# Optimization experiments

Hardware: AMD Instinct MI355X
Metric: run time of the kernel (lower is better)

## Reference

```python
import jax, jax.numpy as jnp
import numpy as np

SQRT_DK = np.sqrt(512.0).astype(np.float32)


def setup_inputs() -> dict:
    key = jax.random.key(0)
    k1, k2, k3 = jax.random.split(key, 3)
    x = jax.random.normal(k1, (16, 2048, 512), dtype=jnp.float32)
    W1 = jax.random.normal(k2, (512, 10), dtype=jnp.float32) * 0.05
    W2 = jax.random.normal(k3, (10, 512), dtype=jnp.float32) * 0.05
    return {"x": x, "W1": W1, "W2": W2}


def reference(x, W1, W2):
    # x: [B, A, D]; low-rank bilinear scores: (x@W1) @ (W2@x^T) -> [B, A, A]
    B, A, D = x.shape
    left = jnp.einsum('bad,dr->bar', x, W1)          # [B, A, 10]
    right = jnp.einsum('rd,bcd->brc', W2, x)         # [B, 10, A]
    scores = jnp.einsum('bar,brc->bac', left, right)  # [B, A, A]
    attn = jax.nn.softmax(scores / SQRT_DK, axis=-1)
    out = jnp.einsum('bac,bcd->bad', attn, x)         # requires_value=True
    return out
```

## Files before the change

### kernel.cpp

```cpp
#include <hip/hip_runtime.h>
#include <cstdint>
#include <cstddef>


typedef float    f32x4 __attribute__((ext_vector_type(4)));
typedef _Float16 half8 __attribute__((ext_vector_type(8)));
typedef _Float16 half4 __attribute__((ext_vector_type(4)));
typedef _Float16 half2 __attribute__((ext_vector_type(2)));

#define B_  16
#define A_  2048
#define D_  512
#define SCALE 0.04419417382415922f

__global__ __launch_bounds__(256) void k01_prep(const float* __restrict__ x,
                                                const float* __restrict__ W1,
                                                const float* __restrict__ W2,
                                                _Float16* __restrict__ xT,
                                                float* __restrict__ left,
                                                _Float16* __restrict__ rightT) {
    __shared__ float xs[64 * 64];
    __shared__ _Float16 Wc[32 * 520];
    int t = threadIdx.x;
    for (int i = t; i < 2560; i += 256) {
        int r = i >> 8, d = (i & 255) << 1;
        half2 h;
        h[0] = (_Float16)(W1[d * 10 + r] * SCALE);
        h[1] = (_Float16)(W1[(d + 1) * 10 + r] * SCALE);
        *(half2*)&Wc[r * 520 + d] = h;
    }
    for (int i = t; i < 2560; i += 256) {
        int r = i >> 8, d = (i & 255) << 1;
        half2 h;
        h[0] = (_Float16)W2[r * 512 + d];
        h[1] = (_Float16)W2[r * 512 + d + 1];
        *(half2*)&Wc[(16 + r) * 520 + d] = h;
    }
    for (int i = t; i < 3120; i += 256) {
        int rz = i / 260, dw = i % 260;
        int row = rz < 6 ? 10 + rz : 20 + rz;
        *(uint32_t*)&Wc[row * 520 + dw * 2] = 0u;
    }

    int bid = blockIdx.x;
    int b = bid >> 5, rg = bid & 31;
    int c0 = rg << 6;
    const float* xb = x + ((size_t)(b * A_ + c0)) * D_;
    int lane = t & 63, w = t >> 6, quad = lane >> 4, col = lane & 15;
    f32x4 accA = {0.f, 0.f, 0.f, 0.f}, accB = {0.f, 0.f, 0.f, 0.f};

    for (int dc = 0; dc < 8; ++dc) {
        int d0 = dc << 6;
        __syncthreads();
#pragma unroll
        for (int j = 0; j < 4; ++j) {
            int idx = t + 256 * j;
            int c = idx >> 4, ch = idx & 15;
            float4 v = *(const float4*)(xb + (size_t)c * D_ + d0 + ch * 4);
            *(float4*)&xs[c * 64 + ((ch ^ (c & 15)) << 2)] = v;
        }
        __syncthreads();
        _Float16* xo = xT + ((size_t)b * D_ + d0) * A_ + c0;
#pragma unroll
        for (int j = 0; j < 4; ++j) {
            int idx = t + 256 * j;
            int d = idx >> 4, cq = (idx & 15) << 2;
            int ch = d >> 2, e = d & 3;
            half4 h;
#pragma unroll
            for (int k = 0; k < 4; ++k) {
                int c = cq + k;
                h[k] = (_Float16)xs[c * 64 + ((ch ^ (c & 15)) << 2) + e];
            }
            *(half4*)(xo + (size_t)d * A_ + cq) = h;
        }
#pragma unroll
        for (int kt = 0; kt < 2; ++kt) {
            int kk = kt * 32 + quad * 8;
            int r = w * 16 + col;
            int ch0 = kk >> 2;
            float4 v0 = *(const float4*)&xs[r * 64 + ((ch0 ^ col) << 2)];
            float4 v1 = *(const float4*)&xs[r * 64 + (((ch0 + 1) ^ col) << 2)];
            half8 af;
            af[0] = (_Float16)v0.x; af[1] = (_Float16)v0.y; af[2] = (_Float16)v0.z; af[3] = (_Float16)v0.w;
            af[4] = (_Float16)v1.x; af[5] = (_Float16)v1.y; af[6] = (_Float16)v1.z; af[7] = (_Float16)v1.w;
            int k = d0 + kk;
            half8 bf0 = *(const half8*)&Wc[col * 520 + k];
            half8 bf1 = *(const half8*)&Wc[(col + 16) * 520 + k];
            accA = __builtin_amdgcn_mfma_f32_16x16x32_f16(af, bf0, accA, 0, 0, 0);
            accB = __builtin_amdgcn_mfma_f32_16x16x32_f16(af, bf1, accB, 0, 0, 0);
        }
    }
#pragma unroll
    for (int q = 0; q < 4; ++q) {
        size_t grow = (size_t)bid * 64 + w * 16 + quad * 4 + q;
        if (col < 10) left[grow * 10 + col] = accA[q];
        if (col < 12) rightT[grow * 12 + col] = (_Float16)accB[q];
    }
}

__global__ __launch_bounds__(256, 2) void k3_attn(const _Float16* __restrict__ xT,
                                                  const float* __restrict__ left,
                                                  const _Float16* __restrict__ rightT,
                                                  float* __restrict__ out) {
    __shared__ _Float16 XTl[256 * 32];
    __shared__ _Float16 Ps[128 * 40];
    __shared__ _Float16 rl[32 * 40];
    __shared__ float rowsum[128];
    int t = threadIdx.x, lane = t & 63, w = t >> 6;
    int quad = lane >> 4, c16 = lane & 15;
    int bid = blockIdx.x;
    int nb = bid & 1, at = (bid >> 1) & 15, b = bid >> 5;
    int a0 = at << 7, n0 = nb << 8;
    int waveM = w & 1, waveN = w >> 1;

    for (int i = t; i < 320; i += 256) {
        int c = i / 10, dw = i % 10;
        *(uint32_t*)((char*)rl + c * 80 + 24 + dw * 4) = 0u;
    }

    half8 lf[2];
#pragma unroll
    for (int i = 0; i < 2; ++i) {
        int arow = a0 + (2 * w + i) * 16 + c16;
        const float* lp = left + (size_t)((b << 11) + arow) * 10;
#pragma unroll
        for (int j = 0; j < 8; ++j) {
            int r = quad * 8 + j;
            lf[i][j] = (r < 10) ? (_Float16)lp[r] : (_Float16)0.f;
        }
    }

    f32x4 acc[4][8];
#pragma unroll
    for (int mi = 0; mi < 4; ++mi)
#pragma unroll
        for (int ni = 0; ni < 8; ++ni) acc[mi][ni] = (f32x4){0.f, 0.f, 0.f, 0.f};
    float psum[2][4] = {{0.f, 0.f, 0.f, 0.f}, {0.f, 0.f, 0.f, 0.f}};

    const _Float16* xTb = xT + ((size_t)b * D_ + n0) * A_;
    const _Float16* rTb = rightT + (size_t)(b << 11) * 12;

    int psA[4];
#pragma unroll
    for (int mi = 0; mi < 4; ++mi) psA[mi] = (waveM * 64 + mi * 16 + c16) * 80 + quad * 16;
    int xtB[8];
#pragma unroll
    for (int ni = 0; ni < 8; ++ni) {
        int nr = waveN * 128 + ni * 16 + c16;
        xtB[ni] = nr * 64 + ((quad ^ ((nr >> 1) & 3)) << 4);
    }
    int rlB[2];
#pragma unroll
    for (int kh = 0; kh < 2; ++kh) rlB[kh] = (kh * 16 + c16) * 80 + quad * 16;

    int nloc0 = w * 64 + (lane >> 2);
    int kq = lane & 3;

    for (int kt = 0; kt < 64; ++kt) {
        int c0 = kt << 5;
        __syncthreads();
        if (t < 192) {
            int c = t / 6, dw = t % 6;
            uint32_t v = *(const uint32_t*)((const char*)(rTb + (size_t)(c0 + c) * 12) + dw * 4);
            *(uint32_t*)((char*)rl + c * 80 + dw * 4) = v;
        }
#pragma unroll
        for (int cc = 0; cc < 4; ++cc) {
            int nl = nloc0 + cc * 16;
            int kqs = kq ^ ((nl >> 1) & 3);
            const _Float16* src = xTb + (size_t)nl * A_ + c0 + kqs * 8;
            _Float16* dst = &XTl[(w * 64 + cc * 16) * 32];
            __builtin_amdgcn_global_load_lds((const __attribute__((address_space(1))) void*)src,
                                             (__attribute__((address_space(3))) void*)dst,
                                             16, 0, 0);
        }
        __syncthreads();
#pragma unroll
        for (int kh = 0; kh < 2; ++kh) {
            half8 bfr = *(const half8*)((const char*)rl + rlB[kh]);
#pragma unroll
            for (int i = 0; i < 2; ++i) {
                f32x4 z = {0.f, 0.f, 0.f, 0.f};
                f32x4 pc = __builtin_amdgcn_mfma_f32_16x16x32_f16(lf[i], bfr, z, 0, 0, 0);
#pragma unroll
                for (int q = 0; q < 4; ++q) {
                    float p = __expf(pc[q]);
                    psum[i][q] += p;
                    Ps[((2 * w + i) * 16 + quad * 4 + q) * 40 + kh * 16 + c16] = (_Float16)p;
                }
            }
        }
        __syncthreads();
        half8 af[4], bf[8];
#pragma unroll
        for (int mi = 0; mi < 4; ++mi) af[mi] = *(const half8*)((const char*)Ps + psA[mi]);
#pragma unroll
        for (int ni = 0; ni < 8; ++ni) bf[ni] = *(const half8*)((const char*)XTl + xtB[ni]);
#pragma unroll
        for (int mi = 0; mi < 4; ++mi)
#pragma unroll
            for (int ni = 0; ni < 8; ++ni)
                acc[mi][ni] = __builtin_amdgcn_mfma_f32_16x16x32_f16(af[mi], bf[ni], acc[mi][ni], 0, 0, 0);
    }

#pragma unroll
    for (int i = 0; i < 2; ++i)
#pragma unroll
        for (int q = 0; q < 4; ++q) {
            float s = psum[i][q];
            s += __shfl_xor(s, 1);
            s += __shfl_xor(s, 2);
            s += __shfl_xor(s, 4);
            s += __shfl_xor(s, 8);
            if (c16 == 0) rowsum[(2 * w + i) * 16 + quad * 4 + q] = s;
        }
    __syncthreads();

    float* ob = out + ((size_t)b * A_ + a0) * D_ + n0;
#pragma unroll
    for (int mi = 0; mi < 4; ++mi) {
#pragma unroll
        for (int q = 0; q < 4; ++q) {
            int ar = waveM * 64 + mi * 16 + quad * 4 + q;
            float sc = 1.0f / rowsum[ar];
#pragma unroll
            for (int ni = 0; ni < 8; ++ni)
                ob[(size_t)ar * D_ + waveN * 128 + ni * 16 + c16] = acc[mi][ni][q] * sc;
        }
    }
}

extern "C" void kernel_launch(void* const* d_in, const int* in_sizes, int n_in,
                              void* d_out, int out_size, void* d_ws, size_t ws_size,
                              hipStream_t stream) {
    const float* x  = (const float*)d_in[0];
    const float* W1 = (const float*)d_in[1];
    const float* W2 = (const float*)d_in[2];
    float* out = (float*)d_out;
    char* ws = (char*)d_ws;
    _Float16* xT    = (_Float16*)ws;
    float*    left  = (float*)(ws + 33554432);
    _Float16* rightT= (_Float16*)(ws + 34865152);

    k01_prep<<<512, 256, 0, stream>>>(x, W1, W2, xT, left, rightT);
    k3_attn<<<512, 256, 0, stream>>>(xT, left, rightT, out);
}
```

Before: 233.7 us.

## Retile attention and prep kernels, prepack weights, use exp2 softmax

Weight conversion moves into a small separate kernel that writes MFMA-ready fp16 fragments. The prep kernel now uses 32-row tiles with a split-K reduction across wave pairs, and the attention kernel uses 128-wide output tiles with 64-column K steps, occupancy 3, and a grid remap to improve L2 locality. The scale is folded into exp2 with log2e, and the Ps buffer is doubled per K half. This gives more blocks and less per-block weight setup, but it recomputes the score MFMAs for each of the four column tiles and adds a third kernel launch.

```diff
diff --git a/kernel.cpp b/kernel.cpp
--- a/kernel.cpp
+++ b/kernel.cpp
@@ -5,117 +5,128 @@
 
 typedef float    f32x4 __attribute__((ext_vector_type(4)));
 typedef _Float16 half8 __attribute__((ext_vector_type(8)));
-typedef _Float16 half4 __attribute__((ext_vector_type(4)));
-typedef _Float16 half2 __attribute__((ext_vector_type(2)));
 
 #define B_  16
 #define A_  2048
 #define D_  512
-#define SCALE 0.04419417382415922f
+#define KSCALE 0.06375872f
+
+__device__ inline float fast_exp2(float v) {
+#if __has_builtin(__builtin_amdgcn_exp2f)
+    return __builtin_amdgcn_exp2f(v);
+#else
+    return __expf(v * 0.6931471805599453f);
+#endif
+}
+
+__global__ __launch_bounds__(256) void kw_prep(const float* __restrict__ W1,
+                                               const float* __restrict__ W2,
+                                               _Float16* __restrict__ Wf) {
+    int pi = blockIdx.x * 256 + threadIdx.x;
+    int kt = pi >> 6, lane = pi & 63;
+    int quad = lane >> 4, col = lane & 15;
+    half8 h1, h2;
+#pragma unroll
+    for (int j = 0; j < 8; ++j) {
+        int d = kt * 32 + quad * 8 + j;
+        h1[j] = (col < 10) ? (_Float16)(W1[d * 10 + col] * KSCALE) : (_Float16)0.f;
+        h2[j] = (col < 12) ? (_Float16)W2[col * 512 + d] : (_Float16)0.f;
+    }
+    *(half8*)(Wf + (size_t)pi * 16) = h1;
+    *(half8*)(Wf + (size_t)pi * 16 + 8) = h2;
+}
 
 __global__ __launch_bounds__(256) void k01_prep(const float* __restrict__ x,
-                                                const float* __restrict__ W1,
-                                                const float* __restrict__ W2,
+                                                const _Float16* __restrict__ Wf,
                                                 _Float16* __restrict__ xT,
                                                 float* __restrict__ left,
                                                 _Float16* __restrict__ rightT) {
-    __shared__ float xs[64 * 64];
-    __shared__ _Float16 Wc[32 * 520];
-    int t = threadIdx.x;
-    for (int i = t; i < 2560; i += 256) {
-        int r = i >> 8, d = (i & 255) << 1;
-        half2 h;
-        h[0] = (_Float16)(W1[d * 10 + r] * SCALE);
-        h[1] = (_Float16)(W1[(d + 1) * 10 + r] * SCALE);
-        *(half2*)&Wc[r * 520 + d] = h;
-    }
-    for (int i = t; i < 2560; i += 256) {
-        int r = i >> 8, d = (i & 255) << 1;
-        half2 h;
-        h[0] = (_Float16)W2[r * 512 + d];
-        h[1] = (_Float16)W2[r * 512 + d + 1];
-        *(half2*)&Wc[(16 + r) * 520 + d] = h;
-    }
-    for (int i = t; i < 3120; i += 256) {
-        int rz = i / 260, dw = i % 260;
-        int row = rz < 6 ? 10 + rz : 20 + rz;
-        *(uint32_t*)&Wc[row * 520 + dw * 2] = 0u;
-    }
-
+    __shared__ float xs[32 * 64];
+    int t = threadIdx.x, lane = t & 63, w = t >> 6;
+    int quad = lane >> 4, c16 = lane & 15;
     int bid = blockIdx.x;
-    int b = bid >> 5, rg = bid & 31;
-    int c0 = rg << 6;
-    const float* xb = x + ((size_t)(b * A_ + c0)) * D_;
-    int lane = t & 63, w = t >> 6, quad = lane >> 4, col = lane & 15;
+    int b = bid >> 6, grp = bid & 63;
+    int c0 = grp << 5;
+    const float* xb = x + ((size_t)b * A_ + c0) * D_;
+    int tile = w >> 1, kki = w & 1;
+    int ar = tile * 16 + c16;
     f32x4 accA = {0.f, 0.f, 0.f, 0.f}, accB = {0.f, 0.f, 0.f, 0.f};
 
     for (int dc = 0; dc < 8; ++dc) {
-        int d0 = dc << 6;
-        __syncthreads();
-#pragma unroll
-        for (int j = 0; j < 4; ++j) {
-            int idx = t + 256 * j;
-            int c = idx >> 4, ch = idx & 15;
-            float4 v = *(const float4*)(xb + (size_t)c * D_ + d0 + ch * 4);
+        __syncthreads();
+#pragma unroll
+        for (int p = 0; p < 2; ++p) {
+            int c = p * 16 + (t >> 4), ch = t & 15;
+            float4 v = *(const float4*)(xb + (size_t)c * D_ + dc * 64 + ch * 4);
             *(float4*)&xs[c * 64 + ((ch ^ (c & 15)) << 2)] = v;
         }
         __syncthreads();
-        _Float16* xo = xT + ((size_t)b * D_ + d0) * A_ + c0;
-#pragma unroll
-        for (int j = 0; j < 4; ++j) {
-            int idx = t + 256 * j;
-            int d = idx >> 4, cq = (idx & 15) << 2;
-            int ch = d >> 2, e = d & 3;
-            half4 h;
-#pragma unroll
-            for (int k = 0; k < 4; ++k) {
-                int c = cq + k;
-                h[k] = (_Float16)xs[c * 64 + ((ch ^ (c & 15)) << 2) + e];
+        {
+            int dloc = t >> 2, c8 = (t & 3) << 3;
+            int ch = dloc >> 2, e = dloc & 3;
+            half8 h;
+#pragma unroll
+            for (int j = 0; j < 8; ++j) {
+                int c = c8 + j;
+                h[j] = (_Float16)xs[c * 64 + ((ch ^ (c & 15)) << 2) + e];
             }
-            *(half4*)(xo + (size_t)d * A_ + cq) = h;
-        }
-#pragma unroll
-        for (int kt = 0; kt < 2; ++kt) {
-            int kk = kt * 32 + quad * 8;
-            int r = w * 16 + col;
-            int ch0 = kk >> 2;
-            float4 v0 = *(const float4*)&xs[r * 64 + ((ch0 ^ col) << 2)];
-            float4 v1 = *(const float4*)&xs[r * 64 + (((ch0 + 1) ^ col) << 2)];
+            *(half8*)(xT + ((size_t)b * D_ + dc * 64 + dloc) * A_ + c0 + c8) = h;
+        }
+        {
+            int kk = kki * 32;
+            int ch0 = (kk >> 2) + quad * 2;
+            float4 v0 = *(const float4*)&xs[ar * 64 + ((ch0 ^ c16) << 2)];
+            float4 v1 = *(const float4*)&xs[ar * 64 + (((ch0 + 1) ^ c16) << 2)];
             half8 af;
             af[0] = (_Float16)v0.x; af[1] = (_Float16)v0.y; af[2] = (_Float16)v0.z; af[3] = (_Float16)v0.w;
             af[4] = (_Float16)v1.x; af[5] = (_Float16)v1.y; af[6] = (_Float16)v1.z; af[7] = (_Float16)v1.w;
-            int k = d0 + kk;
-            half8 bf0 = *(const half8*)&Wc[col * 520 + k];
-            half8 bf1 = *(const half8*)&Wc[(col + 16) * 520 + k];
-            accA = __builtin_amdgcn_mfma_f32_16x16x32_f16(af, bf0, accA, 0, 0, 0);
-            accB = __builtin_amdgcn_mfma_f32_16x16x32_f16(af, bf1, accB, 0, 0, 0);
-        }
-    }
-#pragma unroll
-    for (int q = 0; q < 4; ++q) {
-        size_t grow = (size_t)bid * 64 + w * 16 + quad * 4 + q;
-        if (col < 10) left[grow * 10 + col] = accA[q];
-        if (col < 12) rightT[grow * 12 + col] = (_Float16)accB[q];
-    }
-}
-
-__global__ __launch_bounds__(256, 2) void k3_attn(const _Float16* __restrict__ xT,
+            const half8* wf = (const half8*)(Wf + ((size_t)((dc * 2 + kki) * 64 + lane)) * 16);
+            half8 b1 = wf[0], b2 = wf[1];
+            accA = __builtin_amdgcn_mfma_f32_16x16x32_f16(af, b1, accA, 0, 0, 0);
+            accB = __builtin_amdgcn_mfma_f32_16x16x32_f16(af, b2, accB, 0, 0, 0);
+        }
+    }
+    __syncthreads();
+    float* red = xs;
+    if (kki == 0) {
+#pragma unroll
+        for (int q = 0; q < 4; ++q) {
+            red[tile * 512 + (quad * 4 + q) * 16 + c16] = accA[q];
+            red[tile * 512 + 256 + (quad * 4 + q) * 16 + c16] = accB[q];
+        }
+    }
+    __syncthreads();
+    if (kki == 1) {
+#pragma unroll
+        for (int q = 0; q < 4; ++q) {
+            float a = accA[q] + red[tile * 512 + (quad * 4 + q) * 16 + c16];
+            float bb = accB[q] + red[tile * 512 + 256 + (quad * 4 + q) * 16 + c16];
+            size_t grow = (size_t)bid * 32 + tile * 16 + quad * 4 + q;
+            if (c16 < 10) left[grow * 10 + c16] = a;
+            if (c16 < 12) rightT[grow * 12 + c16] = (_Float16)bb;
+        }
+    }
+}
+
+__global__ __launch_bounds__(256, 3) void k3_attn(const _Float16* __restrict__ xT,
                                                   const float* __restrict__ left,
                                                   const _Float16* __restrict__ rightT,
                                                   float* __restrict__ out) {
-    __shared__ _Float16 XTl[256 * 32];
-    __shared__ _Float16 Ps[128 * 40];
-    __shared__ _Float16 rl[32 * 40];
+    __shared__ _Float16 XTl[128][64];
+    __shared__ _Float16 Ps[2][128][40];
+    __shared__ _Float16 rl[64][40];
     __shared__ float rowsum[128];
     int t = threadIdx.x, lane = t & 63, w = t >> 6;
     int quad = lane >> 4, c16 = lane & 15;
     int bid = blockIdx.x;
-    int nb = bid & 1, at = (bid >> 1) & 15, b = bid >> 5;
-    int a0 = at << 7, n0 = nb << 8;
+    int combo = (bid & 7) | (((bid >> 7) & 7) << 3);
+    int at = (bid >> 3) & 15;
+    int b = combo >> 2, nb = combo & 3;
+    int a0 = at << 7, n0 = nb << 7;
     int waveM = w & 1, waveN = w >> 1;
 
-    for (int i = t; i < 320; i += 256) {
-        int c = i / 10, dw = i % 10;
+    for (int i = t; i < 896; i += 256) {
+        int c = i / 14, dw = i % 14;
         *(uint32_t*)((char*)rl + c * 80 + 24 + dw * 4) = 0u;
     }
 
@@ -131,77 +142,73 @@
         }
     }
 
-    f32x4 acc[4][8];
+    f32x4 acc[4][4];
 #pragma unroll
     for (int mi = 0; mi < 4; ++mi)
 #pragma unroll
-        for (int ni = 0; ni < 8; ++ni) acc[mi][ni] = (f32x4){0.f, 0.f, 0.f, 0.f};
+        for (int ni = 0; ni < 4; ++ni) acc[mi][ni] = (f32x4){0.f, 0.f, 0.f, 0.f};
     float psum[2][4] = {{0.f, 0.f, 0.f, 0.f}, {0.f, 0.f, 0.f, 0.f}};
 
     const _Float16* xTb = xT + ((size_t)b * D_ + n0) * A_;
     const _Float16* rTb = rightT + (size_t)(b << 11) * 12;
 
-    int psA[4];
-#pragma unroll
-    for (int mi = 0; mi < 4; ++mi) psA[mi] = (waveM * 64 + mi * 16 + c16) * 80 + quad * 16;
-    int xtB[8];
-#pragma unroll
-    for (int ni = 0; ni < 8; ++ni) {
-        int nr = waveN * 128 + ni * 16 + c16;
-        xtB[ni] = nr * 64 + ((quad ^ ((nr >> 1) & 3)) << 4);
-    }
-    int rlB[2];
-#pragma unroll
-    for (int kh = 0; kh < 2; ++kh) rlB[kh] = (kh * 16 + c16) * 80 + quad * 16;
-
-    int nloc0 = w * 64 + (lane >> 2);
-    int kq = lane & 3;
-
-    for (int kt = 0; kt < 64; ++kt) {
-        int c0 = kt << 5;
-        __syncthreads();
-        if (t < 192) {
-            int c = t / 6, dw = t % 6;
+    int dmarow = w * 32 + (lane >> 3);
+    int kq = lane & 7;
+
+    for (int kt = 0; kt < 32; ++kt) {
+        int c0 = kt << 6;
+        __syncthreads();
+        for (int i = t; i < 384; i += 256) {
+            int c = i / 6, dw = i % 6;
             uint32_t v = *(const uint32_t*)((const char*)(rTb + (size_t)(c0 + c) * 12) + dw * 4);
             *(uint32_t*)((char*)rl + c * 80 + dw * 4) = v;
         }
 #pragma unroll
         for (int cc = 0; cc < 4; ++cc) {
-            int nl = nloc0 + cc * 16;
-            int kqs = kq ^ ((nl >> 1) & 3);
-            const _Float16* src = xTb + (size_t)nl * A_ + c0 + kqs * 8;
-            _Float16* dst = &XTl[(w * 64 + cc * 16) * 32];
+            int nl = dmarow + cc * 8;
+            const _Float16* src = xTb + (size_t)nl * A_ + c0 + ((kq ^ (nl & 7)) << 3);
+            _Float16* dst = &XTl[w * 32 + cc * 8][0];
             __builtin_amdgcn_global_load_lds((const __attribute__((address_space(1))) void*)src,
                                              (__attribute__((address_space(3))) void*)dst,
                                              16, 0, 0);
         }
         __syncthreads();
 #pragma unroll
-        for (int kh = 0; kh < 2; ++kh) {
-            half8 bfr = *(const half8*)((const char*)rl + rlB[kh]);
-#pragma unroll
-            for (int i = 0; i < 2; ++i) {
-                f32x4 z = {0.f, 0.f, 0.f, 0.f};
-                f32x4 pc = __builtin_amdgcn_mfma_f32_16x16x32_f16(lf[i], bfr, z, 0, 0, 0);
-#pragma unroll
-                for (int q = 0; q < 4; ++q) {
-                    float p = __expf(pc[q]);
-                    psum[i][q] += p;
-                    Ps[((2 * w + i) * 16 + quad * 4 + q) * 40 + kh * 16 + c16] = (_Float16)p;
+        for (int g = 0; g < 2; ++g) {
+#pragma unroll
+            for (int nh = 0; nh < 2; ++nh) {
+                half8 bfr = *(const half8*)((const char*)&rl[g * 32 + nh * 16 + c16][0] + quad * 16);
+#pragma unroll
+                for (int i = 0; i < 2; ++i) {
+                    f32x4 z = {0.f, 0.f, 0.f, 0.f};
+                    f32x4 pc = __builtin_amdgcn_mfma_f32_16x16x32_f16(lf[i], bfr, z, 0, 0, 0);
+#pragma unroll
+                    for (int q = 0; q < 4; ++q) {
+                        float p = fast_exp2(pc[q]);
+                        psum[i][q] += p;
+                        Ps[g][(2 * w + i) * 16 + quad * 4 + q][nh * 16 + c16] = (_Float16)p;
+                    }
                 }
             }
         }
         __syncthreads();
-        half8 af[4], bf[8];
-#pragma unroll
-        for (int mi = 0; mi < 4; ++mi) af[mi] = *(const half8*)((const char*)Ps + psA[mi]);
-#pragma unroll
-        for (int ni = 0; ni < 8; ++ni) bf[ni] = *(const half8*)((const char*)XTl + xtB[ni]);
-#pragma unroll
-        for (int mi = 0; mi < 4; ++mi)
-#pragma unroll
-            for (int ni = 0; ni < 8; ++ni)
-                acc[mi][ni] = __builtin_amdgcn_mfma_f32_16x16x32_f16(af[mi], bf[ni], acc[mi][ni], 0, 0, 0);
+#pragma unroll
+        for (int g = 0; g < 2; ++g) {
+            half8 af[4], bf[4];
+#pragma unroll
+            for (int mi = 0; mi < 4; ++mi)
+                af[mi] = *(const half8*)&Ps[g][waveM * 64 + mi * 16 + c16][quad * 8];
+#pragma unroll
+            for (int ni = 0; ni < 4; ++ni) {
+                int nr = waveN * 64 + ni * 16 + c16;
+                bf[ni] = *(const half8*)&XTl[nr][(((g << 2) + quad) ^ (nr & 7)) << 3];
+            }
+#pragma unroll
+            for (int mi = 0; mi < 4; ++mi)
+#pragma unroll
+                for (int ni = 0; ni < 4; ++ni)
+                    acc[mi][ni] = __builtin_amdgcn_mfma_f32_16x16x32_f16(af[mi], bf[ni], acc[mi][ni], 0, 0, 0);
+        }
     }
 
 #pragma unroll
@@ -225,8 +232,8 @@
             int ar = waveM * 64 + mi * 16 + quad * 4 + q;
             float sc = 1.0f / rowsum[ar];
 #pragma unroll
-            for (int ni = 0; ni < 8; ++ni)
-                ob[(size_t)ar * D_ + waveN * 128 + ni * 16 + c16] = acc[mi][ni][q] * sc;
+            for (int ni = 0; ni < 4; ++ni)
+                ob[(size_t)ar * D_ + waveN * 64 + ni * 16 + c16] = acc[mi][ni][q] * sc;
         }
     }
 }
@@ -242,7 +249,9 @@
     _Float16* xT    = (_Float16*)ws;
     float*    left  = (float*)(ws + 33554432);
     _Float16* rightT= (_Float16*)(ws + 34865152);
-
-    k01_prep<<<512, 256, 0, stream>>>(x, W1, W2, xT, left, rightT);
-    k3_attn<<<512, 256, 0, stream>>>(xT, left, rightT, out);
-}
+    _Float16* Wf    = (_Float16*)(ws + 35651584);
+
+    kw_prep<<<4, 256, 0, stream>>>(W1, W2, Wf);
+    k01_prep<<<1024, 256, 0, stream>>>(x, Wf, xT, left, rightT);
+    k3_attn<<<1024, 256, 0, stream>>>(xT, left, rightT, out);
+}
```

Result: slower. 260.8 us (+11.6%).
